# Kernel optimization log

Measured on AMD Instinct MI355X. Metric: run time of the kernel, lower is better.

Reference implementation:

```python
import jax, jax.numpy as jnp
import numpy as np

D = 4          # simulated tensor-parallel devices (shard_axis size)
B, S = 2, 4096 # batch, seq_len
DIN_S = 512    # per-device input feature shard (full d_model = D*DIN_S = 2048)
DOUT_S = 2048  # per-device output feature shard (full d_out = D*DOUT_S = 8192)


def setup_inputs() -> dict:
    key = jax.random.key(0)
    kx, kw, kb = jax.random.split(key, 3)
    x = jax.random.normal(kx, (D, B, S, DIN_S), dtype=jnp.float32)
    # lecun_normal-style scale: std = 1/sqrt(fan_in) with fan_in = full input dim
    W = jax.random.normal(kw, (D, D, DIN_S, DOUT_S), dtype=jnp.float32) / np.sqrt(D * DIN_S)
    b = jax.random.normal(kb, (D, DOUT_S), dtype=jnp.float32) * 0.01
    return {"x": x, "W": W, "b": b}


def reference(x, W, b):
    # 'gather' TP strategy: device d gathers all input shards x_i and computes
    #   y_d = sum_i x_i @ W[d, i] + b[d]   (bias only added once, by shard idx==0)
    # x: [D, B, S, DIN_S], W: [D_out_dev, D_in_shard, DIN_S, DOUT_S], b: [D, DOUT_S]
    y = jnp.einsum('ibsk,diko->dbso', x, W)  # sum over gathered shards i and k
    return y + b[:, None, None, :]
```

## Files before the change

kernel.cpp:

```cpp
#include <hip/hip_runtime.h>
#include <hip/hip_bf16.h>

#define D_   4
#define M_   8192
#define K_   2048
#define N_   2048
#define DIN  512

typedef __attribute__((ext_vector_type(8))) short  short8v;
typedef __attribute__((ext_vector_type(4))) float  f32x4;

__device__ __forceinline__ unsigned short f2bf(float f) {
  union { float f; unsigned int u; } v; v.f = f;
  unsigned int u = v.u;
  return (unsigned short)((u + 0x7fffu + ((u >> 16) & 1u)) >> 16);
}

__global__ __launch_bounds__(256) void convert_x_kernel(const float* __restrict__ x,
                                                        unsigned short* __restrict__ A) {
  unsigned int tid = blockIdx.x * 256u + threadIdx.x;
  unsigned int kg  = tid & 63u;
  unsigned int i   = (tid >> 6) & 3u;
  unsigned int m   = tid >> 8;
  const float4* src = (const float4*)(x + (size_t)i * ((size_t)M_ * DIN)
                                        + (size_t)m * DIN + (size_t)kg * 8);
  float4 a = src[0];
  float4 b = src[1];
  uint4 pk;
  pk.x = (unsigned int)f2bf(a.x) | ((unsigned int)f2bf(a.y) << 16);
  pk.y = (unsigned int)f2bf(a.z) | ((unsigned int)f2bf(a.w) << 16);
  pk.z = (unsigned int)f2bf(b.x) | ((unsigned int)f2bf(b.y) << 16);
  pk.w = (unsigned int)f2bf(b.z) | ((unsigned int)f2bf(b.w) << 16);
  *(uint4*)(A + (size_t)tid * 8) = pk;
}

__global__ __launch_bounds__(256) void transpose_w_kernel(const float* __restrict__ W,
                                                          unsigned short* __restrict__ Wt) {
  __shared__ float tile[64][65];
  const int d  = blockIdx.z;
  const int k0 = blockIdx.x * 64;
  const int o0 = blockIdx.y * 64;
  const int t  = threadIdx.x;
  const float* src = W + (size_t)d * ((size_t)K_ * N_) + (size_t)k0 * N_ + o0;
  const int c4 = (t & 15) * 4;
  const int r  = t >> 4;
  #pragma unroll
  for (int j = 0; j < 64; j += 16) {
    float4 v = *(const float4*)(src + (size_t)(r + j) * N_ + c4);
    tile[r + j][c4 + 0] = v.x; tile[r + j][c4 + 1] = v.y;
    tile[r + j][c4 + 2] = v.z; tile[r + j][c4 + 3] = v.w;
  }
  __syncthreads();
  unsigned short* dst = Wt + (size_t)d * ((size_t)N_ * K_);
  const int kk = (t & 7) * 8;
  const int oo = t >> 3;
  #pragma unroll
  for (int p = 0; p < 64; p += 32) {
    const int o = oo + p;
    unsigned short tmp[8];
    #pragma unroll
    for (int i = 0; i < 8; i++) tmp[i] = f2bf(tile[kk + i][o]);
    *(uint4*)(dst + (size_t)(o0 + o) * K_ + k0 + kk) = *(uint4*)tmp;
  }
}

#define GLL16(gp, lp)                                                              \
  __builtin_amdgcn_global_load_lds(                                               \
      (const __attribute__((address_space(1))) void*)(gp),                        \
      (__attribute__((address_space(3))) void*)(lp), 16, 0, 0)

__global__ __launch_bounds__(256) void gemm_kernel(const unsigned short* __restrict__ A,
                                                   const unsigned short* __restrict__ Bt,
                                                   const float* __restrict__ bias,
                                                   float* __restrict__ C) {
  __shared__ unsigned short sA[128 * 32];
  __shared__ unsigned short sB[128 * 32];
  const int tid   = threadIdx.x;
  const int wave  = tid >> 6;
  const int lane  = tid & 63;
  const int d     = blockIdx.z;
  const int tileN = blockIdx.x * 128;
  const int tileM = blockIdx.y * 128;

  const int srow = lane >> 2;
  const int scol = ((lane & 3) ^ ((lane >> 3) & 3)) * 8;
  const unsigned short* gA0 = A + (size_t)(tileM + wave * 32 + srow) * K_ + scol;
  const unsigned short* gA1 = gA0 + (size_t)16 * K_;
  const unsigned short* gB0 = Bt + (size_t)d * ((size_t)N_ * K_)
                                 + (size_t)(tileN + wave * 32 + srow) * K_ + scol;
  const unsigned short* gB1 = gB0 + (size_t)16 * K_;
  unsigned short* lA0 = sA + (wave * 32) * 32;
  unsigned short* lA1 = sA + (wave * 32 + 16) * 32;
  unsigned short* lB0 = sB + (wave * 32) * 32;
  unsigned short* lB1 = sB + (wave * 32 + 16) * 32;

  const int wm   = (wave >> 1) * 64;
  const int wn   = (wave & 1) * 64;
  const int fr   = lane & 15;
  const int qw   = lane >> 4;
  const int fcol = (qw ^ ((fr >> 1) & 3)) * 8;

  f32x4 acc[4][4];
  #pragma unroll
  for (int i = 0; i < 4; i++)
    #pragma unroll
    for (int j = 0; j < 4; j++)
      acc[i][j] = (f32x4){0.f, 0.f, 0.f, 0.f};

  for (int k0 = 0; k0 < K_; k0 += 32) {
    GLL16(gA0 + k0, lA0);
    GLL16(gA1 + k0, lA1);
    GLL16(gB0 + k0, lB0);
    GLL16(gB1 + k0, lB1);
    __syncthreads();

    short8v af[4], bfv[4];
    #pragma unroll
    for (int mi = 0; mi < 4; mi++)
      af[mi] = *(const short8v*)(sA + (wm + mi * 16 + fr) * 32 + fcol);
    #pragma unroll
    for (int ni = 0; ni < 4; ni++)
      bfv[ni] = *(const short8v*)(sB + (wn + ni * 16 + fr) * 32 + fcol);
    #pragma unroll
    for (int mi = 0; mi < 4; mi++)
      #pragma unroll
      for (int ni = 0; ni < 4; ni++)
        acc[mi][ni] = __builtin_amdgcn_mfma_f32_16x16x32_bf16(af[mi], bfv[ni],
                                                              acc[mi][ni], 0, 0, 0);
    __syncthreads();
  }

  float* Cd       = C + (size_t)d * ((size_t)M_ * N_);
  const float* bd = bias + d * N_;
  #pragma unroll
  for (int ni = 0; ni < 4; ni++) {
    const int col  = tileN + wn + ni * 16 + fr;
    const float bv = bd[col];
    #pragma unroll
    for (int mi = 0; mi < 4; mi++) {
      const int row0 = tileM + wm + mi * 16 + qw * 4;
      #pragma unroll
      for (int r = 0; r < 4; r++)
        Cd[(size_t)(row0 + r) * N_ + col] = acc[mi][ni][r] + bv;
    }
  }
}

__global__ void naive_kernel(const float* __restrict__ x, const float* __restrict__ W,
                             const float* __restrict__ bias, float* __restrict__ y) {
  long idx = (long)blockIdx.x * blockDim.x + threadIdx.x;
  if (idx >= (long)D_ * M_ * N_) return;
  int  n = (int)(idx % N_);
  long t = idx / N_;
  int  m = (int)(t % M_);
  int  d = (int)(t / M_);
  float acc = bias[d * N_ + n];
  const float* wd = W + (size_t)d * ((size_t)K_ * N_);
  for (int i = 0; i < D_; i++) {
    const float* xr = x + (size_t)i * ((size_t)M_ * DIN) + (size_t)m * DIN;
    const float* wr = wd + (size_t)i * ((size_t)DIN * N_) + n;
    #pragma unroll 4
    for (int k = 0; k < DIN; k++) acc += xr[k] * wr[(size_t)k * N_];
  }
  y[idx] = acc;
}

extern "C" void kernel_launch(void* const* d_in, const int* in_sizes, int n_in,
                              void* d_out, int out_size, void* d_ws, size_t ws_size,
                              hipStream_t stream) {
  const float* x    = (const float*)d_in[0];
  const float* W    = (const float*)d_in[1];
  const float* bias = (const float*)d_in[2];
  float* out        = (float*)d_out;

  const size_t a_elems  = (size_t)M_ * K_;
  const size_t wt_elems = (size_t)D_ * N_ * K_;
  const size_t need     = (a_elems + wt_elems) * sizeof(unsigned short);

  if (ws_size >= need) {
    unsigned short* Abf = (unsigned short*)d_ws;
    unsigned short* Wt  = Abf + a_elems;

    convert_x_kernel<<<(M_ * K_ / 8) / 256, 256, 0, stream>>>(x, Abf);

    dim3 tgrid(K_ / 64, N_ / 64, D_);
    transpose_w_kernel<<<tgrid, 256, 0, stream>>>(W, Wt);

    dim3 ggrid(N_ / 128, M_ / 128, D_);
    gemm_kernel<<<ggrid, 256, 0, stream>>>(Abf, Wt, bias, out);
  } else {
    long total = (long)D_ * M_ * N_;
    naive_kernel<<<(unsigned int)((total + 255) / 256), 256, 0, stream>>>(x, W, bias, out);
  }
}
```

Measured before the change: 649.6 us.

## Double GEMM K-tile to 64 with new LDS swizzle and XCD-aware tile mapping

Raises the per-iteration K step from 32 to 64, so each block loads 128x64 tiles of A and B per barrier pair and runs two MFMA sub-steps between syncs. This halves the number of __syncthreads and global-load round trips. It also adds a new XOR swizzle for the 64-wide rows, and remaps block indices so blocks landing on the same XCD share M rows. The cost is doubled LDS usage and a non-pipelined load, which can still stall on memory.

After: 616.7 us. 5.1% less time.

```diff
diff --git a/kernel.cpp b/kernel.cpp
--- a/kernel.cpp
+++ b/kernel.cpp
@@ -73,32 +73,32 @@
                                                    const unsigned short* __restrict__ Bt,
                                                    const float* __restrict__ bias,
                                                    float* __restrict__ C) {
-  __shared__ unsigned short sA[128 * 32];
-  __shared__ unsigned short sB[128 * 32];
+  __shared__ unsigned short sA[128 * 64];
+  __shared__ unsigned short sB[128 * 64];
   const int tid   = threadIdx.x;
   const int wave  = tid >> 6;
   const int lane  = tid & 63;
   const int d     = blockIdx.z;
-  const int tileN = blockIdx.x * 128;
-  const int tileM = blockIdx.y * 128;
-
-  const int srow = lane >> 2;
-  const int scol = ((lane & 3) ^ ((lane >> 3) & 3)) * 8;
-  const unsigned short* gA0 = A + (size_t)(tileM + wave * 32 + srow) * K_ + scol;
-  const unsigned short* gA1 = gA0 + (size_t)16 * K_;
-  const unsigned short* gB0 = Bt + (size_t)d * ((size_t)N_ * K_)
-                                 + (size_t)(tileN + wave * 32 + srow) * K_ + scol;
-  const unsigned short* gB1 = gB0 + (size_t)16 * K_;
-  unsigned short* lA0 = sA + (wave * 32) * 32;
-  unsigned short* lA1 = sA + (wave * 32 + 16) * 32;
-  unsigned short* lB0 = sB + (wave * 32) * 32;
-  unsigned short* lB1 = sB + (wave * 32 + 16) * 32;
+
+  const int lin   = blockIdx.y * 16 + blockIdx.x;
+  const int xcd   = lin & 7;
+  const int t     = lin >> 3;
+  const int tileN = (xcd * 2 + (t & 1)) * 128;
+  const int tileM = (t >> 1) * 128;
+
+  const int srow = lane >> 3;
+  const int scol = ((lane & 7) ^ srow) * 8;
+  const unsigned short* gA = A + (size_t)(tileM + wave * 32 + srow) * K_ + scol;
+  const unsigned short* gB = Bt + (size_t)d * ((size_t)N_ * K_)
+                                + (size_t)(tileN + wave * 32 + srow) * K_ + scol;
+  unsigned short* lA = sA + (wave * 32) * 64;
+  unsigned short* lB = sB + (wave * 32) * 64;
 
   const int wm   = (wave >> 1) * 64;
   const int wn   = (wave & 1) * 64;
   const int fr   = lane & 15;
   const int qw   = lane >> 4;
-  const int fcol = (qw ^ ((fr >> 1) & 3)) * 8;
+  const int fc0  = (qw ^ (fr & 7)) * 8;
 
   f32x4 acc[4][4];
   #pragma unroll
@@ -107,26 +107,31 @@
     for (int j = 0; j < 4; j++)
       acc[i][j] = (f32x4){0.f, 0.f, 0.f, 0.f};
 
-  for (int k0 = 0; k0 < K_; k0 += 32) {
-    GLL16(gA0 + k0, lA0);
-    GLL16(gA1 + k0, lA1);
-    GLL16(gB0 + k0, lB0);
-    GLL16(gB1 + k0, lB1);
+  for (int k0 = 0; k0 < K_; k0 += 64) {
+    #pragma unroll
+    for (int j = 0; j < 4; j++) {
+      GLL16(gA + (size_t)j * 8 * K_ + k0, lA + j * 8 * 64);
+      GLL16(gB + (size_t)j * 8 * K_ + k0, lB + j * 8 * 64);
+    }
     __syncthreads();
 
-    short8v af[4], bfv[4];
-    #pragma unroll
-    for (int mi = 0; mi < 4; mi++)
-      af[mi] = *(const short8v*)(sA + (wm + mi * 16 + fr) * 32 + fcol);
-    #pragma unroll
-    for (int ni = 0; ni < 4; ni++)
-      bfv[ni] = *(const short8v*)(sB + (wn + ni * 16 + fr) * 32 + fcol);
-    #pragma unroll
-    for (int mi = 0; mi < 4; mi++)
+    #pragma unroll
+    for (int ks = 0; ks < 2; ks++) {
+      const int fc = fc0 ^ (ks * 32);
+      short8v af[4], bfv[4];
+      #pragma unroll
+      for (int mi = 0; mi < 4; mi++)
+        af[mi] = *(const short8v*)(sA + (wm + mi * 16 + fr) * 64 + fc);
       #pragma unroll
       for (int ni = 0; ni < 4; ni++)
-        acc[mi][ni] = __builtin_amdgcn_mfma_f32_16x16x32_bf16(af[mi], bfv[ni],
-                                                              acc[mi][ni], 0, 0, 0);
+        bfv[ni] = *(const short8v*)(sB + (wn + ni * 16 + fr) * 64 + fc);
+      #pragma unroll
+      for (int mi = 0; mi < 4; mi++)
+        #pragma unroll
+        for (int ni = 0; ni < 4; ni++)
+          acc[mi][ni] = __builtin_amdgcn_mfma_f32_16x16x32_bf16(af[mi], bfv[ni],
+                                                                acc[mi][ni], 0, 0, 0);
+    }
     __syncthreads();
   }
 
```
